# Performance work log

Hardware: AMD Instinct MI355X
Metric: run time of the kernel (lower is better)

Reference implementation:

```python
import jax, jax.numpy as jnp
import numpy as np

K = 7           # kernel_size
GROUPS = 16     # channels // group_channels = 256 // 16
GC = 16         # group_channels
BN_EPS = 1e-5


def setup_inputs() -> dict:
    key = jax.random.key(0)
    ks = jax.random.split(key, 6)
    B, C, H, W = 4, 256, 64, 64
    cr = C // 4                      # reduction_ratio = 4
    k2g = K * K * GROUPS             # conv2 out channels = 784
    return {
        "feature_map": jax.random.normal(ks[0], (B, C, H, W), jnp.float32),
        "guide_map":   jax.random.normal(ks[1], (B, C, H, W), jnp.float32),
        "w1": jax.random.normal(ks[2], (cr, C), jnp.float32) * 0.05,
        "bn_gamma": jnp.ones((cr,), jnp.float32),
        "bn_beta":  jnp.zeros((cr,), jnp.float32),
        "bn_mean":  jax.random.normal(ks[3], (cr,), jnp.float32) * 0.1,
        "bn_var":   jax.random.uniform(ks[4], (cr,), jnp.float32, 0.5, 1.5),
        "w2": jax.random.normal(ks[5], (k2g, cr), jnp.float32) * 0.05,
        "b2": jnp.zeros((k2g,), jnp.float32),
    }


def reference(feature_map, guide_map, w1, bn_gamma, bn_beta, bn_mean, bn_var, w2, b2):
    b, c, h, w = feature_map.shape
    # conv1 (1x1) + BN (inference stats) + ReLU
    x = jnp.einsum("oc,bchw->bohw", w1, guide_map)
    inv = bn_gamma / jnp.sqrt(bn_var + BN_EPS)
    x = x * inv[None, :, None, None] + (bn_beta - bn_mean * inv)[None, :, None, None]
    x = jax.nn.relu(x)
    # conv2 (1x1): dynamic per-pixel kernel weights -> [b, groups, k^2, h, w]
    weight = jnp.einsum("oc,bchw->bohw", w2, x) + b2[None, :, None, None]
    weight = weight.reshape(b, GROUPS, K * K, h, w)
    # unfold feature_map (same padding, stride 1) -> [b, c, k^2, h, w]
    pad = (K - 1) // 2
    fp = jnp.pad(feature_map, ((0, 0), (0, 0), (pad, pad), (pad, pad)))
    patches = jnp.stack(
        [fp[:, :, i:i + h, j:j + w] for i in range(K) for j in range(K)], axis=2
    )
    patches = patches.reshape(b, GROUPS, GC, K * K, h, w)
    # dynamic weighted aggregation over kernel positions, then residual
    out = jnp.einsum("bgkhw,bgckhw->bgchw", weight, patches)
    return out.reshape(b, c, h, w) + feature_map
```

## Files before the change

### kernel.cpp

```cpp
#include <hip/hip_runtime.h>

#define BN_EPS 1e-5f

typedef __bf16 bf16_t;
typedef __bf16 bf16x8 __attribute__((ext_vector_type(8)));
typedef __bf16 bf16x4 __attribute__((ext_vector_type(4)));
typedef __bf16 bf16x2 __attribute__((ext_vector_type(2)));
typedef float  floatx4 __attribute__((ext_vector_type(4)));

#define MFMA16(a, b, c) __builtin_amdgcn_mfma_f32_16x16x32_bf16((a), (b), (c), 0, 0, 0)

#define XT_OFF  0
#define WG_OFF  0x200000
#define W1B_OFF 0x1A80000
#define W2B_OFF (0x1A80000 + 32768)
#define B1_OFF  (0x1A80000 + 32768 + 100352)

__global__ __launch_bounds__(256) void prep(
    const float* __restrict__ w1, const float* __restrict__ gamma,
    const float* __restrict__ beta, const float* __restrict__ mean,
    const float* __restrict__ var, const float* __restrict__ w2,
    bf16_t* __restrict__ w1b, bf16_t* __restrict__ w2b, float* __restrict__ bias1)
{
    const int idx = blockIdx.x * 256 + threadIdx.x;
    if (idx < 16384) {
        const int o = idx >> 8;
        const float inv = gamma[o] * rsqrtf(var[o] + BN_EPS);
        w1b[idx] = (bf16_t)(w1[idx] * inv);
        if (idx < 64) {
            const float iv = gamma[idx] * rsqrtf(var[idx] + BN_EPS);
            bias1[idx] = beta[idx] - mean[idx] * iv;
        }
    } else if (idx < 16384 + 50176) {
        const int j = idx - 16384;
        w2b[j] = (bf16_t)w2[j];
    }
}

#define GTP 264

__global__ __launch_bounds__(256) void conv1_k(
    const float* __restrict__ guide, const bf16_t* __restrict__ w1b,
    const float* __restrict__ bias1, bf16_t* __restrict__ xT)
{
    __shared__ __attribute__((aligned(16))) bf16_t gTs[64 * GTP];
    const int b = blockIdx.x >> 6, h = blockIdx.x & 63;
    const int t = threadIdx.x;

    const float* gsrc = guide + (size_t)b * 256 * 4096 + h * 64;
#pragma unroll
    for (int i = 0; i < 32; ++i) {
        const int idx = i * 256 + t;
        const int c2 = idx >> 6, p = idx & 63;
        const float g0 = gsrc[(size_t)(2 * c2) * 4096 + p];
        const float g1 = gsrc[(size_t)(2 * c2 + 1) * 4096 + p];
        bf16x2 pk; pk[0] = (bf16_t)g0; pk[1] = (bf16_t)g1;
        *(bf16x2*)&gTs[p * GTP + 2 * c2] = pk;
    }
    __syncthreads();

    const int wv = t >> 6, ln = t & 63, l15 = ln & 15, q = ln >> 4;
    floatx4 acc[4] = {};
    const bf16_t* ap = w1b + (wv * 16 + l15) * 256;
#pragma unroll
    for (int ks = 0; ks < 8; ++ks) {
        const bf16x8 a = *(const bf16x8*)(ap + ks * 32 + q * 8);
#pragma unroll
        for (int nt = 0; nt < 4; ++nt) {
            const bf16x8 bb = *(const bf16x8*)&gTs[(nt * 16 + l15) * GTP + ks * 32 + q * 8];
            acc[nt] = MFMA16(a, bb, acc[nt]);
        }
    }
    float bi[4];
#pragma unroll
    for (int j = 0; j < 4; ++j) bi[j] = bias1[wv * 16 + q * 4 + j];
#pragma unroll
    for (int nt = 0; nt < 4; ++nt) {
        const int p = nt * 16 + l15;
        bf16x4 v;
#pragma unroll
        for (int j = 0; j < 4; ++j) v[j] = (bf16_t)fmaxf(acc[nt][j] + bi[j], 0.f);
        *(bf16x4*)(xT + ((size_t)(b * 64 + h) * 64 + p) * 64 + wv * 16 + q * 4) = v;
    }
}

#define WTP 136

__global__ __launch_bounds__(256) void conv2_k(
    const bf16_t* __restrict__ xT, const bf16_t* __restrict__ w2b,
    const float* __restrict__ b2, bf16_t* __restrict__ wg)
{
    __shared__ __attribute__((aligned(16))) bf16_t wgt[64 * WTP];
    const int g = blockIdx.x & 15;
    const int bp0 = (blockIdx.x >> 4) * 128;
    const int t = threadIdx.x;
    const int wv = t >> 6, ln = t & 63, l15 = ln & 15, q = ln >> 4;

    floatx4 acc[4][2] = {};
    const bf16_t* brow = xT + (size_t)(bp0 + wv * 32) * 64;
#pragma unroll
    for (int ks = 0; ks < 2; ++ks) {
        bf16x8 bfr[2];
        bfr[0] = *(const bf16x8*)(brow + l15 * 64 + ks * 32 + q * 8);
        bfr[1] = *(const bf16x8*)(brow + (16 + l15) * 64 + ks * 32 + q * 8);
#pragma unroll
        for (int mt = 0; mt < 4; ++mt) {
            int row = mt * 16 + l15; if (row > 48) row = 48;
            const bf16x8 a = *(const bf16x8*)(w2b + (size_t)(g * 49 + row) * 64 + ks * 32 + q * 8);
            acc[mt][0] = MFMA16(a, bfr[0], acc[mt][0]);
            acc[mt][1] = MFMA16(a, bfr[1], acc[mt][1]);
        }
    }
#pragma unroll
    for (int mt = 0; mt < 4; ++mt) {
#pragma unroll
        for (int j = 0; j < 4; ++j) {
            const int k = mt * 16 + q * 4 + j;
            if (k < 49) {
                const float bias = b2[g * 49 + k];
                wgt[k * WTP + wv * 32 + l15]      = (bf16_t)(acc[mt][0][j] + bias);
                wgt[k * WTP + wv * 32 + 16 + l15] = (bf16_t)(acc[mt][1][j] + bias);
            }
        }
    }
    __syncthreads();
    for (int u = t; u < 784; u += 256) {
        const int k = u >> 4, c16 = u & 15;
        *(uint4*)(wg + (size_t)(g * 49 + k) * 16384 + bp0 + c16 * 8) =
            *(const uint4*)&wgt[k * WTP + c16 * 8];
    }
}

#define WGLP 264

__global__ __launch_bounds__(256) void agg_k(
    const bf16_t* __restrict__ wg, const float* __restrict__ feat,
    float* __restrict__ out)
{
    __shared__ __attribute__((aligned(16))) bf16_t wgl[49 * WGLP];
    const int g = blockIdx.x & 15;
    const int rest = blockIdx.x >> 4;
    const int b = rest >> 4, hq = rest & 15;
    const int t = threadIdx.x;

#pragma unroll
    for (int i = 0; i < 7; ++i) {
        const int u = i * 256 + t;
        if (u < 1568) {
            const int k = u >> 5, off = (u & 31) * 8;
            *(uint4*)&wgl[k * WGLP + off] =
                *(const uint4*)(wg + (size_t)(g * 49 + k) * 16384 + b * 4096 + hq * 256 + off);
        }
    }
    __syncthreads();

    const int wq = t & 15, r = (t >> 4) & 3, cp = t >> 6;
    const int w0 = wq * 4;
    const int ch0 = g * 16 + cp * 4;
    const int hr = hq * 4 + r;

    float acc[4][4] = {};
    float4 res[4];
#pragma unroll
    for (int di = 0; di < 7; ++di) {
        const int hh = hr + di - 3;
        if (hh < 0 || hh >= 64) continue;
        float f[4][10];
#pragma unroll
        for (int c = 0; c < 4; ++c) {
            const float* rp = feat + ((size_t)(b * 256 + ch0 + c) * 64 + hh) * 64;
            float4 L = {0, 0, 0, 0}, R = {0, 0, 0, 0};
            if (wq > 0)  L = *(const float4*)(rp + w0 - 4);
            const float4 M = *(const float4*)(rp + w0);
            if (wq < 15) R = *(const float4*)(rp + w0 + 4);
            if (di == 3) res[c] = M;
            f[c][0] = L.y; f[c][1] = L.z; f[c][2] = L.w; f[c][3] = M.x; f[c][4] = M.y;
            f[c][5] = M.z; f[c][6] = M.w; f[c][7] = R.x; f[c][8] = R.y; f[c][9] = R.z;
        }
        const bf16_t* wrow = &wgl[(di * 7) * WGLP + r * 64 + w0];
#pragma unroll
        for (int dj = 0; dj < 7; ++dj) {
            const bf16x4 wb = *(const bf16x4*)(wrow + dj * WGLP);
#pragma unroll
            for (int x = 0; x < 4; ++x) {
                const float wf = (float)wb[x];
#pragma unroll
                for (int c = 0; c < 4; ++c)
                    acc[c][x] = fmaf(wf, f[c][x + dj], acc[c][x]);
            }
        }
    }
#pragma unroll
    for (int c = 0; c < 4; ++c) {
        const size_t ob = ((size_t)(b * 256 + ch0 + c) * 64 + hr) * 64 + w0;
        float4 o;
        o.x = acc[c][0] + res[c].x; o.y = acc[c][1] + res[c].y;
        o.z = acc[c][2] + res[c].z; o.w = acc[c][3] + res[c].w;
        *(float4*)(out + ob) = o;
    }
}

extern "C" void kernel_launch(void* const* d_in, const int* in_sizes, int n_in,
                              void* d_out, int out_size, void* d_ws, size_t ws_size,
                              hipStream_t stream) {
    const float* feature = (const float*)d_in[0];
    const float* guide   = (const float*)d_in[1];
    const float* w1      = (const float*)d_in[2];
    const float* gamma   = (const float*)d_in[3];
    const float* beta    = (const float*)d_in[4];
    const float* mean    = (const float*)d_in[5];
    const float* var     = (const float*)d_in[6];
    const float* w2      = (const float*)d_in[7];
    const float* b2      = (const float*)d_in[8];
    float* out = (float*)d_out;

    char* ws = (char*)d_ws;
    bf16_t* xT    = (bf16_t*)(ws + XT_OFF);
    bf16_t* wg    = (bf16_t*)(ws + WG_OFF);
    bf16_t* w1b   = (bf16_t*)(ws + W1B_OFF);
    bf16_t* w2b   = (bf16_t*)(ws + W2B_OFF);
    float*  bias1 = (float*) (ws + B1_OFF);

    prep<<<260, 256, 0, stream>>>(w1, gamma, beta, mean, var, w2, w1b, w2b, bias1);
    conv1_k<<<256, 256, 0, stream>>>(guide, w1b, bias1, xT);
    conv2_k<<<2048, 256, 0, stream>>>(xT, w2b, b2, wg);
    agg_k<<<1024, 256, 0, stream>>>(wg, feature, out);
}
```

Before: 141.8 us.

## Stage feature halo tile in LDS for aggregation, halve rows per block

The aggregation kernel now loads a zero-padded 16-channel by 8-row by 72-column feature tile into shared memory once per block and reads the 7x7 window from LDS, instead of each thread issuing repeated global float4 loads with boundary branches. Each block now covers 2 output rows instead of 4, so the grid doubles to 2048 blocks and each thread handles 2 channels instead of 4. This cuts redundant global and L2 traffic and branch divergence. In exchange it uses about 50KB of LDS per block, which limits occupancy, and each thread does less work, so per-block setup costs weigh more.

```diff
diff --git a/kernel.cpp b/kernel.cpp
--- a/kernel.cpp
+++ b/kernel.cpp
@@ -131,51 +131,60 @@
     }
 }
 
-#define WGLP 264
+#define FSR 72
+#define FSC 576
+#define WGLP 136
 
 __global__ __launch_bounds__(256) void agg_k(
     const bf16_t* __restrict__ wg, const float* __restrict__ feat,
     float* __restrict__ out)
 {
+    __shared__ __attribute__((aligned(16))) float  fs[16 * FSC];
     __shared__ __attribute__((aligned(16))) bf16_t wgl[49 * WGLP];
+
     const int g = blockIdx.x & 15;
     const int rest = blockIdx.x >> 4;
-    const int b = rest >> 4, hq = rest & 15;
+    const int b = rest >> 5, hp = rest & 31;
+    const int h0 = hp * 2;
     const int t = threadIdx.x;
 
-#pragma unroll
-    for (int i = 0; i < 7; ++i) {
+    for (int u = t; u < 784; u += 256) {
+        const int k = u >> 4, c16 = u & 15;
+        *(uint4*)&wgl[k * WGLP + c16 * 8] =
+            *(const uint4*)(wg + (size_t)(g * 49 + k) * 16384 + b * 4096 + hp * 128 + c16 * 8);
+    }
+#pragma unroll
+    for (int i = 0; i < 9; ++i) {
         const int u = i * 256 + t;
-        if (u < 1568) {
-            const int k = u >> 5, off = (u & 31) * 8;
-            *(uint4*)&wgl[k * WGLP + off] =
-                *(const uint4*)(wg + (size_t)(g * 49 + k) * 16384 + b * 4096 + hq * 256 + off);
-        }
+        const int c = u / 144, rem = u - c * 144;
+        const int rr = rem / 18, qq = rem - rr * 18;
+        const int hh = h0 - 3 + rr;
+        float4 v = {0.f, 0.f, 0.f, 0.f};
+        if (qq >= 1 && qq <= 16 && hh >= 0 && hh < 64)
+            v = *(const float4*)(feat + ((size_t)(b * 256 + g * 16 + c) * 64 + hh) * 64 + (qq - 1) * 4);
+        *(float4*)&fs[c * FSC + rr * FSR + qq * 4] = v;
     }
     __syncthreads();
 
-    const int wq = t & 15, r = (t >> 4) & 3, cp = t >> 6;
+    const int wq = t & 15, r = (t >> 4) & 1, cp = t >> 5;
     const int w0 = wq * 4;
-    const int ch0 = g * 16 + cp * 4;
-    const int hr = hq * 4 + r;
-
-    float acc[4][4] = {};
-    float4 res[4];
+    const int ch0 = cp * 2;
+
+    float acc[2][4] = {};
 #pragma unroll
     for (int di = 0; di < 7; ++di) {
-        const int hh = hr + di - 3;
-        if (hh < 0 || hh >= 64) continue;
-        float f[4][10];
-#pragma unroll
-        for (int c = 0; c < 4; ++c) {
-            const float* rp = feat + ((size_t)(b * 256 + ch0 + c) * 64 + hh) * 64;
-            float4 L = {0, 0, 0, 0}, R = {0, 0, 0, 0};
-            if (wq > 0)  L = *(const float4*)(rp + w0 - 4);
-            const float4 M = *(const float4*)(rp + w0);
-            if (wq < 15) R = *(const float4*)(rp + w0 + 4);
-            if (di == 3) res[c] = M;
-            f[c][0] = L.y; f[c][1] = L.z; f[c][2] = L.w; f[c][3] = M.x; f[c][4] = M.y;
-            f[c][5] = M.z; f[c][6] = M.w; f[c][7] = R.x; f[c][8] = R.y; f[c][9] = R.z;
+        const int ri = r + di;
+        float f0[12], f1[12];
+        {
+            const float* p0 = &fs[ch0 * FSC + ri * FSR + w0];
+            const float* p1 = p0 + FSC;
+#pragma unroll
+            for (int qj = 0; qj < 3; ++qj) {
+                const floatx4 a = *(const floatx4*)(p0 + qj * 4);
+                const floatx4 bq = *(const floatx4*)(p1 + qj * 4);
+#pragma unroll
+                for (int j = 0; j < 4; ++j) { f0[qj * 4 + j] = a[j]; f1[qj * 4 + j] = bq[j]; }
+            }
         }
         const bf16_t* wrow = &wgl[(di * 7) * WGLP + r * 64 + w0];
 #pragma unroll
@@ -184,18 +193,19 @@
 #pragma unroll
             for (int x = 0; x < 4; ++x) {
                 const float wf = (float)wb[x];
-#pragma unroll
-                for (int c = 0; c < 4; ++c)
-                    acc[c][x] = fmaf(wf, f[c][x + dj], acc[c][x]);
+                acc[0][x] = fmaf(wf, f0[x + dj + 1], acc[0][x]);
+                acc[1][x] = fmaf(wf, f1[x + dj + 1], acc[1][x]);
             }
         }
     }
-#pragma unroll
-    for (int c = 0; c < 4; ++c) {
-        const size_t ob = ((size_t)(b * 256 + ch0 + c) * 64 + hr) * 64 + w0;
+
+#pragma unroll
+    for (int c = 0; c < 2; ++c) {
+        const floatx4 res = *(const floatx4*)&fs[(ch0 + c) * FSC + (r + 3) * FSR + 4 + w0];
+        const size_t ob = ((size_t)(b * 256 + g * 16 + ch0 + c) * 64 + h0 + r) * 64 + w0;
         float4 o;
-        o.x = acc[c][0] + res[c].x; o.y = acc[c][1] + res[c].y;
-        o.z = acc[c][2] + res[c].z; o.w = acc[c][3] + res[c].w;
+        o.x = acc[c][0] + res[0]; o.y = acc[c][1] + res[1];
+        o.z = acc[c][2] + res[2]; o.w = acc[c][3] + res[3];
         *(float4*)(out + ob) = o;
     }
 }
@@ -224,5 +234,5 @@
     prep<<<260, 256, 0, stream>>>(w1, gamma, beta, mean, var, w2, w1b, w2b, bias1);
     conv1_k<<<256, 256, 0, stream>>>(guide, w1b, bias1, xT);
     conv2_k<<<2048, 256, 0, stream>>>(xT, w2b, b2, wg);
-    agg_k<<<1024, 256, 0, stream>>>(wg, feature, out);
-}
+    agg_k<<<2048, 256, 0, stream>>>(wg, feature, out);
+}
```

Result: faster. 132.1 us (-6.8%).
